# Kernel optimization log

Measured on AMD Instinct MI355X. Metric: run time of the kernel, lower is better.

## Reference

```python
import jax, jax.numpy as jnp
import numpy as np

ENC_H = 128
DEC_H = 256
DEC_STEPS = 10


def _gru_cell(x, h, Wih, Whh, bih, bhh):
    # PyTorch GRU cell, gate order (r, z, n)
    gi = x @ Wih.T + bih          # (B, 3H)
    gh = h @ Whh.T + bhh          # (B, 3H)
    H = h.shape[-1]
    ir, iz, inn = gi[:, :H], gi[:, H:2 * H], gi[:, 2 * H:]
    hr, hz, hn = gh[:, :H], gh[:, H:2 * H], gh[:, 2 * H:]
    r = jax.nn.sigmoid(ir + hr)
    z = jax.nn.sigmoid(iz + hz)
    n = jnp.tanh(inn + r * hn)
    return (1.0 - z) * n + z * h


def setup_inputs() -> dict:
    key = jax.random.key(0)
    ks = jax.random.split(key, 12)
    B, S = 4096, 128
    s = 0.1
    return {
        "x": jax.random.normal(ks[0], (B, S, 5), jnp.float32),
        "y": jax.random.normal(ks[1], (B, S, 1), jnp.float32),
        "enc_Wih": jax.random.normal(ks[2], (3 * ENC_H, 5), jnp.float32) * s,
        "enc_Whh": jax.random.normal(ks[3], (3 * ENC_H, ENC_H), jnp.float32) * s,
        "enc_bih": jax.random.normal(ks[4], (3 * ENC_H,), jnp.float32) * s,
        "enc_bhh": jax.random.normal(ks[5], (3 * ENC_H,), jnp.float32) * s,
        "dec_Wih": jax.random.normal(ks[6], (3 * DEC_H, ENC_H + 1), jnp.float32) * s,
        "dec_Whh": jax.random.normal(ks[7], (3 * DEC_H, DEC_H), jnp.float32) * s,
        "dec_bih": jax.random.normal(ks[8], (3 * DEC_H,), jnp.float32) * s,
        "dec_bhh": jax.random.normal(ks[9], (3 * DEC_H,), jnp.float32) * s,
        "lin_W": jax.random.normal(ks[10], (4, DEC_H), jnp.float32) * s,
        "lin_b": jax.random.normal(ks[11], (4,), jnp.float32) * s,
    }


def reference(x, y, enc_Wih, enc_Whh, enc_bih, enc_bhh,
              dec_Wih, dec_Whh, dec_bih, dec_bhh, lin_W, lin_b):
    B, S, _ = x.shape
    xs = jnp.transpose(x, (1, 0, 2))   # (S, B, 5)
    ys = jnp.transpose(y, (1, 0, 2))   # (S, B, 1)

    # Encoder: only the final hidden state (contex) is consumed downstream.
    h0 = jnp.zeros((B, ENC_H), x.dtype)

    def enc_step(h, xt):
        return _gru_cell(xt, h, enc_Wih, enc_Whh, enc_bih, enc_bhh), None

    contex, _ = jax.lax.scan(enc_step, h0, xs)   # (B, 128)

    # Decoder: initial hidden is ones (torch.ones_like(shape)), 10 steps.
    hdec0 = jnp.ones((B, DEC_H), x.dtype)

    def dec_step(h, yt):
        xt = jnp.concatenate([contex, yt], axis=-1)   # (B, 129)
        h2 = _gru_cell(xt, h, dec_Wih, dec_Whh, dec_bih, dec_bhh)
        out = h2 @ lin_W.T + lin_b                    # (B, 4)
        return h2, out

    _, outs = jax.lax.scan(dec_step, hdec0, ys[:DEC_STEPS])  # (10, B, 4)

    # res starts as ones; only first 10 rows written.
    res = jnp.ones((S, B, 4), x.dtype).at[:DEC_STEPS].set(outs)
    return jnp.transpose(res, (1, 0, 2))   # (B, S, 4)
```

## Files before the change

kernel.cpp:

```cpp
#include <hip/hip_runtime.h>

#define B_SZ 4096
#define S_SZ 128
#define XD 5
#define EH 128
#define DH 256
#define DSTEPS 10

typedef short v8s __attribute__((ext_vector_type(8)));
typedef float v4f __attribute__((ext_vector_type(4)));

__device__ __forceinline__ float bf2f(unsigned short u) {
    union { unsigned int i; float f; } v; v.i = ((unsigned int)u) << 16; return v.f;
}
__device__ __forceinline__ unsigned short f2bf(float f) {
    union { float f; unsigned int i; } v; v.f = f;
    unsigned int x = v.i;
    return (unsigned short)((x + 0x7FFFu + ((x >> 16) & 1u)) >> 16);
}
__device__ __forceinline__ float fexp2(float x) { return __builtin_amdgcn_exp2f(x); }
__device__ __forceinline__ float frcp(float x) { return __builtin_amdgcn_rcpf(x); }
__device__ __forceinline__ float sigmoidf_(float x) {
    return frcp(1.f + fexp2(-1.44269504088896f * x));
}
__device__ __forceinline__ float tanhf_(float x) {
    float e = fexp2(2.88539008177793f * x);
    return 1.f - 2.f * frcp(e + 1.f);
}

__global__ __launch_bounds__(512) void enc_kernel(
    const float* __restrict__ x,
    const float* __restrict__ Wih32,
    const float* __restrict__ Whh32,
    const float* __restrict__ bih,
    const float* __restrict__ bhh,
    const float* __restrict__ dWih,
    const float* __restrict__ dWhh,
    unsigned short* __restrict__ wihp,
    unsigned short* __restrict__ dWhh_bf,
    unsigned short* __restrict__ ctex)
{
    __shared__ unsigned short xs[S_SZ][16][8];
    __shared__ unsigned short hb[2][16][136];
    __shared__ unsigned short zpad[8];

    const int tid = threadIdx.x;
    const int bid = blockIdx.x;
    const int wv = tid >> 6;
    const int lane = tid & 63;
    const int n = lane & 15;
    const int kg = lane >> 4;
    const int r0 = bid * 16;

    for (int i = bid * 512 + tid; i < 768 * 256; i += 131072)
        dWhh_bf[i] = f2bf(dWhh[i]);
    for (int i = bid * 512 + tid; i < 768 * 136; i += 131072) {
        int col = i / 136, k = i - col * 136;
        wihp[i] = (k < 129) ? f2bf(dWih[col * 129 + k]) : (unsigned short)0;
    }

    for (int i = tid; i < 2 * 16 * 136; i += 512) ((unsigned short*)hb)[i] = 0;
    if (tid < 8) zpad[tid] = 0;
    for (int i = tid; i < 16 * S_SZ * 8; i += 512) {
        int m = i >> 10;
        int rem = i & 1023;
        int t = rem >> 3;
        int j = rem & 7;
        unsigned short v = 0;
        if (j < XD) v = f2bf(x[(size_t)(r0 + m) * (S_SZ * XD) + t * XD + j]);
        xs[t][m][j] = v;
    }

    const int colw = wv * 16 + n;
    v8s fw[3][4];
    v8s fx[3];
    #pragma unroll
    for (int g = 0; g < 3; ++g) {
        int gcol = g * EH + colw;
        #pragma unroll
        for (int kt = 0; kt < 4; ++kt) {
            const float* p = &Whh32[(size_t)gcol * EH + kt * 32 + kg * 8];
            float4 lo = *(const float4*)p;
            float4 hi = *(const float4*)(p + 4);
            v8s f;
            f[0] = (short)f2bf(lo.x); f[1] = (short)f2bf(lo.y);
            f[2] = (short)f2bf(lo.z); f[3] = (short)f2bf(lo.w);
            f[4] = (short)f2bf(hi.x); f[5] = (short)f2bf(hi.y);
            f[6] = (short)f2bf(hi.z); f[7] = (short)f2bf(hi.w);
            fw[g][kt] = f;
        }
        v8s t = {0, 0, 0, 0, 0, 0, 0, 0};
        if (kg == 0) {
            const float* p = &Wih32[gcol * XD];
            #pragma unroll
            for (int j = 0; j < XD; ++j) t[j] = (short)f2bf(p[j]);
        }
        fx[g] = t;
    }
    const float b_r  = bih[colw]          + bhh[colw];
    const float b_z  = bih[EH + colw]     + bhh[EH + colw];
    const float bi_n = bih[2 * EH + colw];
    const float bh_n = bhh[2 * EH + colw];

    float hst[4] = {0.f, 0.f, 0.f, 0.f};
    __syncthreads();

    #pragma unroll 2
    for (int t = 0; t < S_SZ; ++t) {
        const int p = t & 1;
        v8s a[4];
        #pragma unroll
        for (int kt = 0; kt < 4; ++kt)
            a[kt] = *(const v8s*)&hb[p][n][kt * 32 + kg * 8];
        const unsigned short* xsrc = (kg == 0) ? &xs[t][n][0] : &zpad[0];
        v8s ax = *(const v8s*)xsrc;

        v4f accr  = {b_r, b_r, b_r, b_r};
        v4f accz  = {b_z, b_z, b_z, b_z};
        v4f acchn = {bh_n, bh_n, bh_n, bh_n};
        v4f accin = {bi_n, bi_n, bi_n, bi_n};
        #pragma unroll
        for (int kt = 0; kt < 4; ++kt) {
            accr  = __builtin_amdgcn_mfma_f32_16x16x32_bf16(a[kt], fw[0][kt], accr, 0, 0, 0);
            accz  = __builtin_amdgcn_mfma_f32_16x16x32_bf16(a[kt], fw[1][kt], accz, 0, 0, 0);
            acchn = __builtin_amdgcn_mfma_f32_16x16x32_bf16(a[kt], fw[2][kt], acchn, 0, 0, 0);
        }
        accr  = __builtin_amdgcn_mfma_f32_16x16x32_bf16(ax, fx[0], accr, 0, 0, 0);
        accz  = __builtin_amdgcn_mfma_f32_16x16x32_bf16(ax, fx[1], accz, 0, 0, 0);
        accin = __builtin_amdgcn_mfma_f32_16x16x32_bf16(ax, fx[2], accin, 0, 0, 0);

        #pragma unroll
        for (int e = 0; e < 4; ++e) {
            float r = sigmoidf_(accr[e]);
            float z = sigmoidf_(accz[e]);
            float nn = tanhf_(accin[e] + r * acchn[e]);
            float h = (1.f - z) * nn + z * hst[e];
            hst[e] = h;
            hb[1 - p][kg * 4 + e][colw] = f2bf(h);
        }
        __syncthreads();
    }
    #pragma unroll
    for (int e = 0; e < 4; ++e)
        ctex[(size_t)(r0 + kg * 4 + e) * EH + colw] = f2bf(hst[e]);
}

__global__ __launch_bounds__(512)
__attribute__((amdgpu_waves_per_eu(2, 2)))
void dec_all_kernel(
    const unsigned short* __restrict__ dWhh_bf,
    const unsigned short* __restrict__ wihp,
    const float* __restrict__ dbih,
    const float* __restrict__ dbhh,
    const float* __restrict__ y,
    const unsigned short* __restrict__ ctex,
    const float* __restrict__ linW,
    const float* __restrict__ linb,
    float* __restrict__ out)
{
    __shared__ unsigned short wshn[32 * 264 * 8];
    __shared__ unsigned short hshf[32 * 16 * 8];
    __shared__ unsigned short lwf[32 * 16 * 8];

    const int tid  = threadIdx.x;
    const int w    = tid >> 6;
    const int lane = tid & 63;
    const int n    = lane & 15;
    const int kg   = lane >> 4;
    const int rb   = blockIdx.x * 16;
    const int cbase = w * 32;

    for (int i = tid; i < 256 * 32; i += 512) {
        int col = i >> 5, kgrp = i & 31;
        uint4 v = *(const uint4*)&dWhh_bf[(size_t)(512 + col) * 256 + kgrp * 8];
        *(uint4*)&wshn[(kgrp * 264 + col) * 8] = v;
    }
    {
        int col = tid >> 5, kgrp = tid & 31;
        unsigned short v8[8];
        #pragma unroll
        for (int j = 0; j < 8; ++j)
            v8[j] = (col < 4) ? f2bf(linW[col * 256 + kgrp * 8 + j]) : (unsigned short)0;
        *(uint4*)&lwf[(kgrp * 16 + col) * 8] = *(uint4*)v8;
    }
    for (int i = tid; i < 32 * 16 * 8; i += 512) hshf[i] = 0x3F80;

    v8s fB[2][2][8];
    #pragma unroll
    for (int g = 0; g < 2; ++g)
        #pragma unroll
        for (int cg = 0; cg < 2; ++cg)
            #pragma unroll
            for (int kt = 0; kt < 8; ++kt)
                fB[g][cg][kt] = *(const v8s*)
                    &dWhh_bf[(size_t)(g * DH + cbase + cg * 16 + n) * DH + kt * 32 + kg * 8];

    v4f gi[3][2];
    float wy[3][2], bNh[2];
    #pragma unroll
    for (int g = 0; g < 3; ++g)
        #pragma unroll
        for (int cg = 0; cg < 2; ++cg) {
            int gcol = g * DH + cbase + cg * 16 + n;
            float bb = dbih[gcol] + ((g < 2) ? dbhh[gcol] : 0.f);
            gi[g][cg] = (v4f){bb, bb, bb, bb};
            wy[g][cg] = bf2f(wihp[(size_t)gcol * 136 + 128]);
        }
    #pragma unroll
    for (int cg = 0; cg < 2; ++cg)
        bNh[cg] = dbhh[2 * DH + cbase + cg * 16 + n];

    #pragma unroll
    for (int kt = 0; kt < 4; ++kt) {
        v8s a = *(const v8s*)&ctex[(size_t)(rb + n) * EH + kt * 32 + kg * 8];
        #pragma unroll
        for (int g = 0; g < 3; ++g)
            #pragma unroll
            for (int cg = 0; cg < 2; ++cg) {
                v8s b = *(const v8s*)
                    &wihp[(size_t)(g * DH + cbase + cg * 16 + n) * 136 + kt * 32 + kg * 8];
                gi[g][cg] = __builtin_amdgcn_mfma_f32_16x16x32_bf16(a, b, gi[g][cg], 0, 0, 0);
            }
    }

    const float lb = (n < 4) ? linb[n] : 0.f;
    float hprev[2][4];
    #pragma unroll
    for (int cg = 0; cg < 2; ++cg)
        #pragma unroll
        for (int e = 0; e < 4; ++e) hprev[cg][e] = 1.0f;

    __syncthreads();

    for (int t = 0; t < DSTEPS; ++t) {
        float yv[4];
        #pragma unroll
        for (int e = 0; e < 4; ++e)
            yv[e] = y[(size_t)(rb + kg * 4 + e) * S_SZ + t];

        v4f ar[2], az[2], an[2];
        #pragma unroll
        for (int cg = 0; cg < 2; ++cg) {
            ar[cg] = (v4f){0.f, 0.f, 0.f, 0.f};
            az[cg] = (v4f){0.f, 0.f, 0.f, 0.f};
            an[cg] = (v4f){bNh[cg], bNh[cg], bNh[cg], bNh[cg]};
        }
        #pragma unroll
        for (int kt = 0; kt < 8; ++kt) {
            v8s a = *(const v8s*)&hshf[((kt * 4 + kg) * 16 + n) * 8];
            #pragma unroll
            for (int cg = 0; cg < 2; ++cg) {
                v8s bn_ = *(const v8s*)&wshn[((kt * 4 + kg) * 264 + cbase + cg * 16 + n) * 8];
                ar[cg] = __builtin_amdgcn_mfma_f32_16x16x32_bf16(a, fB[0][cg][kt], ar[cg], 0, 0, 0);
                az[cg] = __builtin_amdgcn_mfma_f32_16x16x32_bf16(a, fB[1][cg][kt], az[cg], 0, 0, 0);
                an[cg] = __builtin_amdgcn_mfma_f32_16x16x32_bf16(a, bn_,           an[cg], 0, 0, 0);
            }
        }
        __syncthreads();

        #pragma unroll
        for (int cg = 0; cg < 2; ++cg) {
            const int chi = 4 * w + 2 * cg + (n >> 3);
            #pragma unroll
            for (int e = 0; e < 4; ++e) {
                float r  = sigmoidf_(gi[0][cg][e] + yv[e] * wy[0][cg] + ar[cg][e]);
                float z  = sigmoidf_(gi[1][cg][e] + yv[e] * wy[1][cg] + az[cg][e]);
                float nn = tanhf_(gi[2][cg][e] + yv[e] * wy[2][cg] + r * an[cg][e]);
                float h  = nn + z * (hprev[cg][e] - nn);
                hprev[cg][e] = h;
                hshf[(chi * 16 + kg * 4 + e) * 8 + (n & 7)] = f2bf(h);
            }
        }
        __syncthreads();

        if (w == 0) {
            v4f o4 = {0.f, 0.f, 0.f, 0.f};
            #pragma unroll
            for (int kt = 0; kt < 8; ++kt) {
                v8s a = *(const v8s*)&hshf[((kt * 4 + kg) * 16 + n) * 8];
                v8s b = *(const v8s*)&lwf[((kt * 4 + kg) * 16 + n) * 8];
                o4 = __builtin_amdgcn_mfma_f32_16x16x32_bf16(a, b, o4, 0, 0, 0);
            }
            if (n < 4) {
                #pragma unroll
                for (int e = 0; e < 4; ++e)
                    out[(size_t)(rb + kg * 4 + e) * (S_SZ * 4) + t * 4 + n] = o4[e] + lb;
            }
        }
    }

    for (int j = tid; j < 16 * 512; j += 512) {
        int row = j >> 9, c = j & 511;
        if (c >= DSTEPS * 4) out[(size_t)(rb + row) * 512 + c] = 1.0f;
    }
}

extern "C" void kernel_launch(void* const* d_in, const int* in_sizes, int n_in,
                              void* d_out, int out_size, void* d_ws, size_t ws_size,
                              hipStream_t stream)
{
    const float* x    = (const float*)d_in[0];
    const float* y    = (const float*)d_in[1];
    const float* eWih = (const float*)d_in[2];
    const float* eWhh = (const float*)d_in[3];
    const float* ebih = (const float*)d_in[4];
    const float* ebhh = (const float*)d_in[5];
    const float* dWih = (const float*)d_in[6];
    const float* dWhh = (const float*)d_in[7];
    const float* dbih = (const float*)d_in[8];
    const float* dbhh = (const float*)d_in[9];
    const float* linW = (const float*)d_in[10];
    const float* linb = (const float*)d_in[11];
    float* out = (float*)d_out;

    char* ws = (char*)d_ws;
    unsigned short* wihp    = (unsigned short*)(ws);
    unsigned short* dWhh_bf = (unsigned short*)(ws + 208896);
    unsigned short* ctex    = (unsigned short*)(ws + 602112);

    enc_kernel<<<256, 512, 0, stream>>>(x, eWih, eWhh, ebih, ebhh,
                                        dWih, dWhh, wihp, dWhh_bf, ctex);
    dec_all_kernel<<<256, 512, 0, stream>>>(dWhh_bf, wihp, dbih, dbhh, y,
                                            ctex, linW, linb, out);
}
```

Measured before the change: 217.0 us.

## Split encoder into 8-row blocks with lane-shuffled gate math and prescaled weights

The encoder now runs 512 blocks of 256 threads, each handling 8 batch rows. Each wave computes 32 hidden columns across two MFMA column groups. Upper-half lanes fetch the second group's accumulators via ds_bpermute, so the gate nonlinearities are split across lanes rather than done redundantly. The sigmoid and tanh exp2 scale factors are folded into the bf16 weights and biases, which removes multiplies from the per-step chain. The cost is that half of each 16-row MFMA tile is zero padding, doubling matrix work per row. Rounding the pre-scaled weights to bf16 also shifts numerics slightly.

```diff
diff --git a/kernel.cpp b/kernel.cpp
--- a/kernel.cpp
+++ b/kernel.cpp
@@ -27,8 +27,13 @@
     float e = fexp2(2.88539008177793f * x);
     return 1.f - 2.f * frcp(e + 1.f);
 }
-
-__global__ __launch_bounds__(512) void enc_kernel(
+__device__ __forceinline__ float pull_x32(float v, int bpaddr) {
+    union { float f; int i; } u; u.f = v;
+    u.i = __builtin_amdgcn_ds_bpermute(bpaddr, u.i);
+    return u.f;
+}
+
+__global__ __launch_bounds__(256, 2) void enc_kernel(
     const float* __restrict__ x,
     const float* __restrict__ Wih32,
     const float* __restrict__ Whh32,
@@ -40,9 +45,9 @@
     unsigned short* __restrict__ dWhh_bf,
     unsigned short* __restrict__ ctex)
 {
-    __shared__ unsigned short xs[S_SZ][16][8];
+    __shared__ unsigned short xs[S_SZ][8][8];
     __shared__ unsigned short hb[2][16][136];
-    __shared__ unsigned short zpad[8];
+    __shared__ __align__(16) unsigned short zpad[8];
 
     const int tid = threadIdx.x;
     const int bid = blockIdx.x;
@@ -50,18 +55,20 @@
     const int lane = tid & 63;
     const int n = lane & 15;
     const int kg = lane >> 4;
-    const int r0 = bid * 16;
-
-    for (int i = bid * 512 + tid; i < 768 * 256; i += 131072)
+    const int r0 = bid * 8;
+    const int cbase = wv * 32;
+    const int bpaddr = (lane ^ 32) << 2;
+
+    for (int i = bid * 256 + tid; i < 768 * 256; i += 131072)
         dWhh_bf[i] = f2bf(dWhh[i]);
-    for (int i = bid * 512 + tid; i < 768 * 136; i += 131072) {
+    for (int i = bid * 256 + tid; i < 768 * 136; i += 131072) {
         int col = i / 136, k = i - col * 136;
         wihp[i] = (k < 129) ? f2bf(dWih[col * 129 + k]) : (unsigned short)0;
     }
 
-    for (int i = tid; i < 2 * 16 * 136; i += 512) ((unsigned short*)hb)[i] = 0;
+    for (int i = tid; i < 2 * 16 * 136; i += 256) ((unsigned short*)hb)[i] = 0;
     if (tid < 8) zpad[tid] = 0;
-    for (int i = tid; i < 16 * S_SZ * 8; i += 512) {
+    for (int i = tid; i < 8 * S_SZ * 8; i += 256) {
         int m = i >> 10;
         int rem = i & 1023;
         int t = rem >> 3;
@@ -71,36 +78,48 @@
         xs[t][m][j] = v;
     }
 
-    const int colw = wv * 16 + n;
-    v8s fw[3][4];
-    v8s fx[3];
+    v8s fw[3][2][4];
+    v8s fx[3][2];
     #pragma unroll
     for (int g = 0; g < 3; ++g) {
-        int gcol = g * EH + colw;
-        #pragma unroll
-        for (int kt = 0; kt < 4; ++kt) {
-            const float* p = &Whh32[(size_t)gcol * EH + kt * 32 + kg * 8];
-            float4 lo = *(const float4*)p;
-            float4 hi = *(const float4*)(p + 4);
-            v8s f;
-            f[0] = (short)f2bf(lo.x); f[1] = (short)f2bf(lo.y);
-            f[2] = (short)f2bf(lo.z); f[3] = (short)f2bf(lo.w);
-            f[4] = (short)f2bf(hi.x); f[5] = (short)f2bf(hi.y);
-            f[6] = (short)f2bf(hi.z); f[7] = (short)f2bf(hi.w);
-            fw[g][kt] = f;
-        }
-        v8s t = {0, 0, 0, 0, 0, 0, 0, 0};
-        if (kg == 0) {
-            const float* p = &Wih32[gcol * XD];
-            #pragma unroll
-            for (int j = 0; j < XD; ++j) t[j] = (short)f2bf(p[j]);
-        }
-        fx[g] = t;
-    }
-    const float b_r  = bih[colw]          + bhh[colw];
-    const float b_z  = bih[EH + colw]     + bhh[EH + colw];
-    const float bi_n = bih[2 * EH + colw];
-    const float bh_n = bhh[2 * EH + colw];
+        const float sc = (g < 2) ? -1.44269504088896f : 2.88539008177793f;
+        #pragma unroll
+        for (int cg = 0; cg < 2; ++cg) {
+            const int gcol = g * EH + cbase + cg * 16 + n;
+            #pragma unroll
+            for (int kt = 0; kt < 4; ++kt) {
+                const float* p = &Whh32[(size_t)gcol * EH + kt * 32 + kg * 8];
+                float4 lo = *(const float4*)p;
+                float4 hi = *(const float4*)(p + 4);
+                v8s f;
+                f[0] = (short)f2bf(sc * lo.x); f[1] = (short)f2bf(sc * lo.y);
+                f[2] = (short)f2bf(sc * lo.z); f[3] = (short)f2bf(sc * lo.w);
+                f[4] = (short)f2bf(sc * hi.x); f[5] = (short)f2bf(sc * hi.y);
+                f[6] = (short)f2bf(sc * hi.z); f[7] = (short)f2bf(sc * hi.w);
+                fw[g][cg][kt] = f;
+            }
+            v8s tv = {0, 0, 0, 0, 0, 0, 0, 0};
+            if (kg == 0) {
+                const float* p = &Wih32[gcol * XD];
+                #pragma unroll
+                for (int j = 0; j < XD; ++j) tv[j] = (short)f2bf(sc * p[j]);
+            }
+            fx[g][cg] = tv;
+        }
+    }
+    float br[2], bz[2], bin_[2], bhn[2];
+    #pragma unroll
+    for (int cg = 0; cg < 2; ++cg) {
+        const int c0 = cbase + cg * 16 + n;
+        br[cg]   = -1.44269504088896f * (bih[c0] + bhh[c0]);
+        bz[cg]   = -1.44269504088896f * (bih[EH + c0] + bhh[EH + c0]);
+        bin_[cg] =  2.88539008177793f * bih[2 * EH + c0];
+        bhn[cg]  =  2.88539008177793f * bhh[2 * EH + c0];
+    }
+
+    const int hi_half = kg >> 1;
+    const int colw = cbase + hi_half * 16 + n;
+    const int rquad = (kg & 1) * 4;
 
     float hst[4] = {0.f, 0.f, 0.f, 0.f};
     __syncthreads();
@@ -112,37 +131,55 @@
         #pragma unroll
         for (int kt = 0; kt < 4; ++kt)
             a[kt] = *(const v8s*)&hb[p][n][kt * 32 + kg * 8];
-        const unsigned short* xsrc = (kg == 0) ? &xs[t][n][0] : &zpad[0];
+        const unsigned short* xsrc = (kg == 0 && n < 8) ? &xs[t][n][0] : &zpad[0];
         v8s ax = *(const v8s*)xsrc;
 
-        v4f accr  = {b_r, b_r, b_r, b_r};
-        v4f accz  = {b_z, b_z, b_z, b_z};
-        v4f acchn = {bh_n, bh_n, bh_n, bh_n};
-        v4f accin = {bi_n, bi_n, bi_n, bi_n};
+        v4f accr[2], accz[2], acchn[2], accin[2];
+        #pragma unroll
+        for (int cg = 0; cg < 2; ++cg) {
+            accr[cg]  = (v4f){br[cg], br[cg], br[cg], br[cg]};
+            accz[cg]  = (v4f){bz[cg], bz[cg], bz[cg], bz[cg]};
+            acchn[cg] = (v4f){bhn[cg], bhn[cg], bhn[cg], bhn[cg]};
+            accin[cg] = (v4f){bin_[cg], bin_[cg], bin_[cg], bin_[cg]};
+        }
         #pragma unroll
         for (int kt = 0; kt < 4; ++kt) {
-            accr  = __builtin_amdgcn_mfma_f32_16x16x32_bf16(a[kt], fw[0][kt], accr, 0, 0, 0);
-            accz  = __builtin_amdgcn_mfma_f32_16x16x32_bf16(a[kt], fw[1][kt], accz, 0, 0, 0);
-            acchn = __builtin_amdgcn_mfma_f32_16x16x32_bf16(a[kt], fw[2][kt], acchn, 0, 0, 0);
-        }
-        accr  = __builtin_amdgcn_mfma_f32_16x16x32_bf16(ax, fx[0], accr, 0, 0, 0);
-        accz  = __builtin_amdgcn_mfma_f32_16x16x32_bf16(ax, fx[1], accz, 0, 0, 0);
-        accin = __builtin_amdgcn_mfma_f32_16x16x32_bf16(ax, fx[2], accin, 0, 0, 0);
+            #pragma unroll
+            for (int cg = 0; cg < 2; ++cg) {
+                accr[cg]  = __builtin_amdgcn_mfma_f32_16x16x32_bf16(a[kt], fw[0][cg][kt], accr[cg], 0, 0, 0);
+                accz[cg]  = __builtin_amdgcn_mfma_f32_16x16x32_bf16(a[kt], fw[1][cg][kt], accz[cg], 0, 0, 0);
+                acchn[cg] = __builtin_amdgcn_mfma_f32_16x16x32_bf16(a[kt], fw[2][cg][kt], acchn[cg], 0, 0, 0);
+            }
+        }
+        #pragma unroll
+        for (int cg = 0; cg < 2; ++cg) {
+            accr[cg]  = __builtin_amdgcn_mfma_f32_16x16x32_bf16(ax, fx[0][cg], accr[cg], 0, 0, 0);
+            accz[cg]  = __builtin_amdgcn_mfma_f32_16x16x32_bf16(ax, fx[1][cg], accz[cg], 0, 0, 0);
+            accin[cg] = __builtin_amdgcn_mfma_f32_16x16x32_bf16(ax, fx[2][cg], accin[cg], 0, 0, 0);
+        }
 
         #pragma unroll
         for (int e = 0; e < 4; ++e) {
-            float r = sigmoidf_(accr[e]);
-            float z = sigmoidf_(accz[e]);
-            float nn = tanhf_(accin[e] + r * acchn[e]);
-            float h = (1.f - z) * nn + z * hst[e];
+            float tr  = pull_x32(accr[1][e],  bpaddr);
+            float tz  = pull_x32(accz[1][e],  bpaddr);
+            float thn = pull_x32(acchn[1][e], bpaddr);
+            float tin = pull_x32(accin[1][e], bpaddr);
+            float vr  = hi_half ? tr  : accr[0][e];
+            float vz  = hi_half ? tz  : accz[0][e];
+            float vhn = hi_half ? thn : acchn[0][e];
+            float vin = hi_half ? tin : accin[0][e];
+            float r  = frcp(1.f + fexp2(vr));
+            float z  = frcp(1.f + fexp2(vz));
+            float nn = 1.f - 2.f * frcp(fexp2(vin + r * vhn) + 1.f);
+            float h  = nn + z * (hst[e] - nn);
             hst[e] = h;
-            hb[1 - p][kg * 4 + e][colw] = f2bf(h);
+            hb[1 - p][rquad + e][colw] = f2bf(h);
         }
         __syncthreads();
     }
     #pragma unroll
     for (int e = 0; e < 4; ++e)
-        ctex[(size_t)(r0 + kg * 4 + e) * EH + colw] = f2bf(hst[e]);
+        ctex[(size_t)(r0 + rquad + e) * EH + colw] = f2bf(hst[e]);
 }
 
 __global__ __launch_bounds__(512)
@@ -318,7 +355,7 @@
     unsigned short* dWhh_bf = (unsigned short*)(ws + 208896);
     unsigned short* ctex    = (unsigned short*)(ws + 602112);
 
-    enc_kernel<<<256, 512, 0, stream>>>(x, eWih, eWhh, ebih, ebhh,
+    enc_kernel<<<512, 256, 0, stream>>>(x, eWih, eWhh, ebih, ebhh,
                                         dWih, dWhh, wihp, dWhh_bf, ctex);
     dec_all_kernel<<<256, 512, 0, stream>>>(dWhh_bf, wihp, dbih, dbhh, y,
                                             ctex, linW, linb, out);
```

Result: slower. 254.5 us (+17.3%).

## Fold activation log2 scales and biases into bf16 weights, cache y in LDS

Applied to the files above, without the earlier changes.

The -log2(e) and 2*log2(e) scaling for sigmoid and tanh is folded into the bf16 encoder and decoder weights and biases at conversion time. In the encoder, the gate biases move into the input MFMA through a constant-one column in x, which removes per-element multiplies and bias setup in the recurrent loop. The encoder packs hidden-state conversion with v_cvt_pk_bf16_f32. The decoder caches its 10 y steps in shared memory and changes the wshn LDS padding stride from 264 to 258. Scaling weights before bf16 rounding changes numerics slightly, and the new LDS stride may change bank conflicts.

```diff
diff --git a/kernel.cpp b/kernel.cpp
--- a/kernel.cpp
+++ b/kernel.cpp
@@ -20,13 +20,14 @@
 }
 __device__ __forceinline__ float fexp2(float x) { return __builtin_amdgcn_exp2f(x); }
 __device__ __forceinline__ float frcp(float x) { return __builtin_amdgcn_rcpf(x); }
-__device__ __forceinline__ float sigmoidf_(float x) {
-    return frcp(1.f + fexp2(-1.44269504088896f * x));
-}
-__device__ __forceinline__ float tanhf_(float x) {
-    float e = fexp2(2.88539008177793f * x);
-    return 1.f - 2.f * frcp(e + 1.f);
-}
+__device__ __forceinline__ unsigned int cvt2bf(float lo, float hi) {
+    unsigned int r;
+    asm("v_cvt_pk_bf16_f32 %0, %1, %2" : "=v"(r) : "v"(lo), "v"(hi));
+    return r;
+}
+
+#define SC_S (-1.44269504088896f)
+#define SC_T ( 2.88539008177793f)
 
 __global__ __launch_bounds__(512) void enc_kernel(
     const float* __restrict__ x,
@@ -42,7 +43,7 @@
 {
     __shared__ unsigned short xs[S_SZ][16][8];
     __shared__ unsigned short hb[2][16][136];
-    __shared__ unsigned short zpad[8];
+    __shared__ __align__(16) unsigned short zpad[8];
 
     const int tid = threadIdx.x;
     const int bid = blockIdx.x;
@@ -52,11 +53,14 @@
     const int kg = lane >> 4;
     const int r0 = bid * 16;
 
-    for (int i = bid * 512 + tid; i < 768 * 256; i += 131072)
-        dWhh_bf[i] = f2bf(dWhh[i]);
+    for (int i = bid * 512 + tid; i < 768 * 256; i += 131072) {
+        const float sc = ((i >> 8) < 512) ? SC_S : SC_T;
+        dWhh_bf[i] = f2bf(sc * dWhh[i]);
+    }
     for (int i = bid * 512 + tid; i < 768 * 136; i += 131072) {
         int col = i / 136, k = i - col * 136;
-        wihp[i] = (k < 129) ? f2bf(dWih[col * 129 + k]) : (unsigned short)0;
+        const float sc = (col < 512) ? SC_S : SC_T;
+        wihp[i] = (k < 129) ? f2bf(sc * dWih[col * 129 + k]) : (unsigned short)0;
     }
 
     for (int i = tid; i < 2 * 16 * 136; i += 512) ((unsigned short*)hb)[i] = 0;
@@ -68,6 +72,7 @@
         int j = rem & 7;
         unsigned short v = 0;
         if (j < XD) v = f2bf(x[(size_t)(r0 + m) * (S_SZ * XD) + t * XD + j]);
+        else if (j == XD) v = 0x3F80;
         xs[t][m][j] = v;
     }
 
@@ -76,32 +81,34 @@
     v8s fx[3];
     #pragma unroll
     for (int g = 0; g < 3; ++g) {
-        int gcol = g * EH + colw;
+        const float sc = (g < 2) ? SC_S : SC_T;
+        const int gcol = g * EH + colw;
         #pragma unroll
         for (int kt = 0; kt < 4; ++kt) {
             const float* p = &Whh32[(size_t)gcol * EH + kt * 32 + kg * 8];
             float4 lo = *(const float4*)p;
             float4 hi = *(const float4*)(p + 4);
             v8s f;
-            f[0] = (short)f2bf(lo.x); f[1] = (short)f2bf(lo.y);
-            f[2] = (short)f2bf(lo.z); f[3] = (short)f2bf(lo.w);
-            f[4] = (short)f2bf(hi.x); f[5] = (short)f2bf(hi.y);
-            f[6] = (short)f2bf(hi.z); f[7] = (short)f2bf(hi.w);
+            f[0] = (short)f2bf(sc * lo.x); f[1] = (short)f2bf(sc * lo.y);
+            f[2] = (short)f2bf(sc * lo.z); f[3] = (short)f2bf(sc * lo.w);
+            f[4] = (short)f2bf(sc * hi.x); f[5] = (short)f2bf(sc * hi.y);
+            f[6] = (short)f2bf(sc * hi.z); f[7] = (short)f2bf(sc * hi.w);
             fw[g][kt] = f;
         }
         v8s t = {0, 0, 0, 0, 0, 0, 0, 0};
         if (kg == 0) {
             const float* p = &Wih32[gcol * XD];
             #pragma unroll
-            for (int j = 0; j < XD; ++j) t[j] = (short)f2bf(p[j]);
+            for (int j = 0; j < XD; ++j) t[j] = (short)f2bf(sc * p[j]);
+            float b = (g < 2) ? (sc * (bih[gcol] + bhh[gcol]))
+                              : (sc * bih[gcol]);
+            t[XD] = (short)f2bf(b);
         }
         fx[g] = t;
     }
-    const float b_r  = bih[colw]          + bhh[colw];
-    const float b_z  = bih[EH + colw]     + bhh[EH + colw];
-    const float bi_n = bih[2 * EH + colw];
-    const float bh_n = bhh[2 * EH + colw];
-
+    const float bhn = SC_T * bhh[2 * EH + colw];
+
+    const v4f vzero = {0.f, 0.f, 0.f, 0.f};
     float hst[4] = {0.f, 0.f, 0.f, 0.f};
     __syncthreads();
 
@@ -115,29 +122,35 @@
         const unsigned short* xsrc = (kg == 0) ? &xs[t][n][0] : &zpad[0];
         v8s ax = *(const v8s*)xsrc;
 
-        v4f accr  = {b_r, b_r, b_r, b_r};
-        v4f accz  = {b_z, b_z, b_z, b_z};
-        v4f acchn = {bh_n, bh_n, bh_n, bh_n};
-        v4f accin = {bi_n, bi_n, bi_n, bi_n};
-        #pragma unroll
-        for (int kt = 0; kt < 4; ++kt) {
+        v4f accr  = __builtin_amdgcn_mfma_f32_16x16x32_bf16(a[0], fw[0][0], vzero, 0, 0, 0);
+        v4f accz  = __builtin_amdgcn_mfma_f32_16x16x32_bf16(a[0], fw[1][0], vzero, 0, 0, 0);
+        v4f acchn = __builtin_amdgcn_mfma_f32_16x16x32_bf16(a[0], fw[2][0], vzero, 0, 0, 0);
+        #pragma unroll
+        for (int kt = 1; kt < 4; ++kt) {
             accr  = __builtin_amdgcn_mfma_f32_16x16x32_bf16(a[kt], fw[0][kt], accr, 0, 0, 0);
             accz  = __builtin_amdgcn_mfma_f32_16x16x32_bf16(a[kt], fw[1][kt], accz, 0, 0, 0);
             acchn = __builtin_amdgcn_mfma_f32_16x16x32_bf16(a[kt], fw[2][kt], acchn, 0, 0, 0);
         }
-        accr  = __builtin_amdgcn_mfma_f32_16x16x32_bf16(ax, fx[0], accr, 0, 0, 0);
-        accz  = __builtin_amdgcn_mfma_f32_16x16x32_bf16(ax, fx[1], accz, 0, 0, 0);
-        accin = __builtin_amdgcn_mfma_f32_16x16x32_bf16(ax, fx[2], accin, 0, 0, 0);
-
+        accr = __builtin_amdgcn_mfma_f32_16x16x32_bf16(ax, fx[0], accr, 0, 0, 0);
+        accz = __builtin_amdgcn_mfma_f32_16x16x32_bf16(ax, fx[1], accz, 0, 0, 0);
+        v4f accin = __builtin_amdgcn_mfma_f32_16x16x32_bf16(ax, fx[2], vzero, 0, 0, 0);
+
+        float hnew[4];
         #pragma unroll
         for (int e = 0; e < 4; ++e) {
-            float r = sigmoidf_(accr[e]);
-            float z = sigmoidf_(accz[e]);
-            float nn = tanhf_(accin[e] + r * acchn[e]);
-            float h = (1.f - z) * nn + z * hst[e];
+            float r  = frcp(1.f + fexp2(accr[e]));
+            float z  = frcp(1.f + fexp2(accz[e]));
+            float nn = 1.f - 2.f * frcp(fexp2(accin[e] + r * (acchn[e] + bhn)) + 1.f);
+            float h  = nn + z * (hst[e] - nn);
             hst[e] = h;
-            hb[1 - p][kg * 4 + e][colw] = f2bf(h);
-        }
+            hnew[e] = h;
+        }
+        const unsigned int pk01 = cvt2bf(hnew[0], hnew[1]);
+        const unsigned int pk23 = cvt2bf(hnew[2], hnew[3]);
+        hb[1 - p][kg * 4 + 0][colw] = (unsigned short)(pk01 & 0xFFFFu);
+        hb[1 - p][kg * 4 + 1][colw] = (unsigned short)(pk01 >> 16);
+        hb[1 - p][kg * 4 + 2][colw] = (unsigned short)(pk23 & 0xFFFFu);
+        hb[1 - p][kg * 4 + 3][colw] = (unsigned short)(pk23 >> 16);
         __syncthreads();
     }
     #pragma unroll
@@ -158,9 +171,10 @@
     const float* __restrict__ linb,
     float* __restrict__ out)
 {
-    __shared__ unsigned short wshn[32 * 264 * 8];
+    __shared__ unsigned short wshn[32 * 258 * 8];
     __shared__ unsigned short hshf[32 * 16 * 8];
     __shared__ unsigned short lwf[32 * 16 * 8];
+    __shared__ float ysh[16][DSTEPS];
 
     const int tid  = threadIdx.x;
     const int w    = tid >> 6;
@@ -173,7 +187,7 @@
     for (int i = tid; i < 256 * 32; i += 512) {
         int col = i >> 5, kgrp = i & 31;
         uint4 v = *(const uint4*)&dWhh_bf[(size_t)(512 + col) * 256 + kgrp * 8];
-        *(uint4*)&wshn[(kgrp * 264 + col) * 8] = v;
+        *(uint4*)&wshn[(kgrp * 258 + col) * 8] = v;
     }
     {
         int col = tid >> 5, kgrp = tid & 31;
@@ -183,6 +197,10 @@
             v8[j] = (col < 4) ? f2bf(linW[col * 256 + kgrp * 8 + j]) : (unsigned short)0;
         *(uint4*)&lwf[(kgrp * 16 + col) * 8] = *(uint4*)v8;
     }
+    if (tid < 16 * DSTEPS) {
+        int row = tid / DSTEPS, tt = tid - row * DSTEPS;
+        ysh[row][tt] = y[(size_t)(rb + row) * S_SZ + tt];
+    }
     for (int i = tid; i < 32 * 16 * 8; i += 512) hshf[i] = 0x3F80;
 
     v8s fB[2][2][8];
@@ -202,13 +220,14 @@
         #pragma unroll
         for (int cg = 0; cg < 2; ++cg) {
             int gcol = g * DH + cbase + cg * 16 + n;
-            float bb = dbih[gcol] + ((g < 2) ? dbhh[gcol] : 0.f);
+            const float sc = (g < 2) ? SC_S : SC_T;
+            float bb = sc * (dbih[gcol] + ((g < 2) ? dbhh[gcol] : 0.f));
             gi[g][cg] = (v4f){bb, bb, bb, bb};
             wy[g][cg] = bf2f(wihp[(size_t)gcol * 136 + 128]);
         }
     #pragma unroll
     for (int cg = 0; cg < 2; ++cg)
-        bNh[cg] = dbhh[2 * DH + cbase + cg * 16 + n];
+        bNh[cg] = SC_T * dbhh[2 * DH + cbase + cg * 16 + n];
 
     #pragma unroll
     for (int kt = 0; kt < 4; ++kt) {
@@ -236,7 +255,7 @@
         float yv[4];
         #pragma unroll
         for (int e = 0; e < 4; ++e)
-            yv[e] = y[(size_t)(rb + kg * 4 + e) * S_SZ + t];
+            yv[e] = ysh[kg * 4 + e][t];
 
         v4f ar[2], az[2], an[2];
         #pragma unroll
@@ -250,7 +269,7 @@
             v8s a = *(const v8s*)&hshf[((kt * 4 + kg) * 16 + n) * 8];
             #pragma unroll
             for (int cg = 0; cg < 2; ++cg) {
-                v8s bn_ = *(const v8s*)&wshn[((kt * 4 + kg) * 264 + cbase + cg * 16 + n) * 8];
+                v8s bn_ = *(const v8s*)&wshn[((kt * 4 + kg) * 258 + cbase + cg * 16 + n) * 8];
                 ar[cg] = __builtin_amdgcn_mfma_f32_16x16x32_bf16(a, fB[0][cg][kt], ar[cg], 0, 0, 0);
                 az[cg] = __builtin_amdgcn_mfma_f32_16x16x32_bf16(a, fB[1][cg][kt], az[cg], 0, 0, 0);
                 an[cg] = __builtin_amdgcn_mfma_f32_16x16x32_bf16(a, bn_,           an[cg], 0, 0, 0);
@@ -263,9 +282,10 @@
             const int chi = 4 * w + 2 * cg + (n >> 3);
             #pragma unroll
             for (int e = 0; e < 4; ++e) {
-                float r  = sigmoidf_(gi[0][cg][e] + yv[e] * wy[0][cg] + ar[cg][e]);
-                float z  = sigmoidf_(gi[1][cg][e] + yv[e] * wy[1][cg] + az[cg][e]);
-                float nn = tanhf_(gi[2][cg][e] + yv[e] * wy[2][cg] + r * an[cg][e]);
+                float r  = frcp(1.f + fexp2(gi[0][cg][e] + yv[e] * wy[0][cg] + ar[cg][e]));
+                float z  = frcp(1.f + fexp2(gi[1][cg][e] + yv[e] * wy[1][cg] + az[cg][e]));
+                float nn = 1.f - 2.f * frcp(
+                    fexp2(gi[2][cg][e] + yv[e] * wy[2][cg] + r * an[cg][e]) + 1.f);
                 float h  = nn + z * (hprev[cg][e] - nn);
                 hprev[cg][e] = h;
                 hshf[(chi * 16 + kg * 4 + e) * 8 + (n & 7)] = f2bf(h);
```

After: 203.2 us. 6.3% less time.
